# Optimization experiments

Measured on AMD Instinct MI355X. Metric: run time of the kernel, lower is better.

## Reference

```python
import jax, jax.numpy as jnp
import numpy as np

B, N, L = 16, 512, 512          # batch, compound atoms, protein words
DIM = 10                         # compound feature dim
DM, H, DK, DFF = 128, 8, 16, 512 # transformer dims
LG, LO = 3, 3                    # layer_gnn, layer_output
NFP, NW = 10000, 10000           # vocab sizes
NEG = -9e15                      # GAT mask sentinel (matches torch code)


def _layernorm(x, g, b, eps=1e-6):
    # annotated-transformer LayerNorm: unbiased std, eps added to std
    m = jnp.mean(x, -1, keepdims=True)
    s = jnp.std(x, -1, keepdims=True, ddof=1)
    return g * (x - m) / (s + eps) + b


def _pos_encoding(length, d_model):
    pos = np.arange(length)[:, None]
    div = np.exp(np.arange(0, d_model, 2) * (-np.log(10000.0) / d_model))
    pe = np.zeros((length, d_model), np.float32)
    pe[:, 0::2] = np.sin(pos * div)
    pe[:, 1::2] = np.cos(pos * div)
    return jnp.asarray(pe)


def setup_inputs():
    ks = iter(jax.random.split(jax.random.key(0), 64))
    def nrm(shape, scale):
        return jax.random.normal(next(ks), shape, jnp.float32) * scale
    return dict(
        fingerprints=jax.random.randint(next(ks), (B, N), 0, NFP, jnp.int32),
        fp_mask=jnp.ones((B, N), jnp.float32),
        adjacency=jax.random.randint(next(ks), (B, N, N), 0, 2, jnp.int32),
        words=jax.random.randint(next(ks), (B, L), 0, NW, jnp.int32),
        words_mask=jnp.ones((B, L), jnp.float32),
        emb_fp=nrm((NFP, DIM), 0.1),
        emb_word=nrm((NW, DM), 0.1),
        Wg=nrm((LG, DIM, DIM), 0.3), bg=jnp.zeros((LG, DIM), jnp.float32),
        attn_a=nrm((LG, 2 * DIM), 0.3),
        Wq=nrm((DM, DM), 0.09), bq=jnp.zeros((DM,), jnp.float32),
        Wk=nrm((DM, DM), 0.09), bk=jnp.zeros((DM,), jnp.float32),
        Wv=nrm((DM, DM), 0.09), bv=jnp.zeros((DM,), jnp.float32),
        Wo=nrm((DM, DM), 0.09), bo=jnp.zeros((DM,), jnp.float32),
        ln1_g=jnp.ones((DM,), jnp.float32), ln1_b=jnp.zeros((DM,), jnp.float32),
        ln2_g=jnp.ones((DM,), jnp.float32), ln2_b=jnp.zeros((DM,), jnp.float32),
        lnf_g=jnp.ones((DM,), jnp.float32), lnf_b=jnp.zeros((DM,), jnp.float32),
        W1=nrm((DM, DFF), 0.09), b1=jnp.zeros((DFF,), jnp.float32),
        W2=nrm((DFF, DM), 0.045), b2=jnp.zeros((DM,), jnp.float32),
        Wtout=nrm((DM, DIM), 0.09), btout=jnp.zeros((DIM,), jnp.float32),
        Watt=nrm((DIM, DIM), 0.3), batt=jnp.zeros((DIM,), jnp.float32),
        Wout=nrm((LO, 2 * DIM, 2 * DIM), 0.2), bout=jnp.zeros((LO, 2 * DIM), jnp.float32),
        Wint=nrm((2 * DIM, 2), 0.2), bint=jnp.zeros((2,), jnp.float32),
    )


def _forward(fingerprints, fp_mask, adjacency, words, words_mask,
             emb_fp, emb_word, Wg, bg, attn_a,
             Wq, bq, Wk, bk, Wv, bv, Wo, bo,
             ln1_g, ln1_b, ln2_g, ln2_b, lnf_g, lnf_b,
             W1, b1, W2, b2, Wtout, btout,
             Watt, batt, Wout, bout, Wint, bint):
    # ---- GAT over compound graph (dropout disabled = eval/deterministic) ----
    xs = emb_fp[fingerprints]                     # [B,N,DIM]
    mask = fp_mask[:, :, None]                    # [B,N,1]
    adj = adjacency > 0
    for i in range(LG):
        h = jax.nn.relu(xs @ Wg[i] + bg[i]) * mask
        # e[b,i,j] = leaky_relu(a1.h_i + a2.h_j)  == leaky_relu([h_i||h_j] @ a)
        s1 = h @ attn_a[i, :DIM]                  # [B,N]
        s2 = h @ attn_a[i, DIM:]                  # [B,N]
        e = jax.nn.leaky_relu(s1[:, :, None] + s2[:, None, :])  # [B,N,N]
        att = jax.nn.softmax(jnp.where(adj, e, NEG), axis=2)
        xs = xs + att @ h
    compound = jnp.mean(xs * mask, axis=1, keepdims=True)       # [B,1,DIM]

    # ---- transformer encoder, 1 layer, annotated-transformer (pre-norm) ----
    x = emb_word[words] * jnp.sqrt(jnp.float32(DM)) + _pos_encoding(L, DM)
    m4 = words_mask[:, None, None, :] > 0         # [B,1,1,L]
    xn = _layernorm(x, ln1_g, ln1_b)
    heads = lambda t: t.reshape(B, L, H, DK).transpose(0, 2, 1, 3)
    q, k, v = heads(xn @ Wq + bq), heads(xn @ Wk + bk), heads(xn @ Wv + bv)
    scores = jnp.einsum('bhqd,bhkd->bhqk', q, k) / jnp.sqrt(jnp.float32(DK))
    p = jax.nn.softmax(jnp.where(m4, scores, -1e9), axis=-1)
    attn = jnp.einsum('bhqk,bhkd->bhqd', p, v).transpose(0, 2, 1, 3).reshape(B, L, DM)
    x = x + (attn @ Wo + bo)
    xn = _layernorm(x, ln2_g, ln2_b)
    x = x + (jax.nn.relu(xn @ W1 + b1) @ W2 + b2)
    x = _layernorm(x, lnf_g, lnf_b)
    word_vectors = jax.nn.relu(x) @ Wtout + btout  # [B,L,DIM]

    # ---- tanh cross-attention (attention_cnn) ----
    hc = jax.nn.relu(compound @ Watt + batt)       # [B,1,DIM]
    hp = jax.nn.relu(word_vectors @ Watt + batt)   # [B,L,DIM]
    w = jnp.tanh(jnp.einsum('bxd,bld->bxl', hc, hp))  # [B,1,L]
    protein = jnp.mean(w.transpose(0, 2, 1) * hp, axis=1, keepdims=True)  # [B,1,DIM]

    cat = jnp.concatenate([compound, protein], axis=2)  # [B,1,2*DIM]
    for j in range(LO):
        cat = jax.nn.relu(cat @ Wout[j] + bout[j])
    return jnp.squeeze(cat @ Wint + bint, axis=1)        # [B,2]


def reference(fingerprints, fp_mask, adjacency, words, words_mask,
              emb_fp, emb_word, Wg, bg, attn_a,
              Wq, bq, Wk, bk, Wv, bv, Wo, bo,
              ln1_g, ln1_b, ln2_g, ln2_b, lnf_g, lnf_b,
              W1, b1, W2, b2, Wtout, btout,
              Watt, batt, Wout, bout, Wint, bint):
    return _forward(fingerprints, fp_mask, adjacency, words, words_mask,
                    emb_fp, emb_word, Wg, bg, attn_a,
                    Wq, bq, Wk, bk, Wv, bv, Wo, bo,
                    ln1_g, ln1_b, ln2_g, ln2_b, lnf_g, lnf_b,
                    W1, b1, W2, b2, Wtout, btout,
                    Watt, batt, Wout, bout, Wint, bint)
```

## Files before the change

kernel.cpp:

```cpp
#include <hip/hip_runtime.h>
#include <hip/hip_bf16.h>
#include <math.h>

#define B 16
#define N 512
#define L 512
#define DIM 10
#define DM 128
#define H 8
#define DK 16
#define DFF 512
#define LG 3
#define LO 3
#define NEGV -9.0e15f
#define RF 16
#define AQR 64

__device__ __forceinline__ float wave_reduce_sum(float v) {
    #pragma unroll
    for (int o = 32; o > 0; o >>= 1) v += __shfl_down(v, o, 64);
    return v;
}

__device__ __forceinline__ float quad_sum(float x) {
    int y1 = __builtin_amdgcn_mov_dpp(__float_as_int(x), 0xB1, 0xF, 0xF, true);
    float s = x + __int_as_float(y1);
    int y2 = __builtin_amdgcn_mov_dpp(__float_as_int(s), 0x4E, 0xF, 0xF, true);
    return s + __int_as_float(y2);
}

__device__ __forceinline__ float half_reduce_sum(float v) {
    #pragma unroll
    for (int o = 16; o > 0; o >>= 1) v += __shfl_xor(v, o, 64);
    return v;
}


__global__ void k_embed_fp(const int* __restrict__ fing, const float* __restrict__ emb_fp,
                           float* __restrict__ xs) {
    int idx = blockIdx.x * blockDim.x + threadIdx.x;
    if (idx >= B * N * DIM) return;
    int d = idx % DIM;
    int bn = idx / DIM;
    xs[idx] = emb_fp[fing[bn] * DIM + d];
}

__global__ void k_gnn_h(const float* __restrict__ xs, const float* __restrict__ fp_mask,
                        const float* __restrict__ Wg, const float* __restrict__ bg,
                        const float* __restrict__ aatt,
                        float* __restrict__ h, float* __restrict__ s1, float* __restrict__ s2) {
    int bn = blockIdx.x * blockDim.x + threadIdx.x;
    if (bn >= B * N) return;
    float x[DIM];
    #pragma unroll
    for (int d = 0; d < DIM; d++) x[d] = xs[bn * DIM + d];
    float m = fp_mask[bn];
    float a1 = 0.f, a2 = 0.f;
    #pragma unroll
    for (int j = 0; j < DIM; j++) {
        float acc = bg[j];
        #pragma unroll
        for (int d = 0; d < DIM; d++) acc += x[d] * Wg[d * DIM + j];
        acc = fmaxf(acc, 0.f) * m;
        h[bn * DIM + j] = acc;
        a1 += acc * aatt[j];
        a2 += acc * aatt[DIM + j];
    }
    s1[bn] = a1;
    s2[bn] = a2;
}

__global__ void k_gnn_att(const float* __restrict__ h, const float* __restrict__ s1,
                          const float* __restrict__ s2, const int* __restrict__ adj,
                          float* __restrict__ xs) {
    int b  = blockIdx.x / (N / 16);
    int rg = blockIdx.x % (N / 16);
    int t = threadIdx.x;
    int g  = t >> 4;
    int ll = t & 15;
    int i = rg * 16 + g;

    __shared__ float h_s[N * DIM];
    __shared__ float s2_s[N];

    const float* hb = h + (long)b * N * DIM;
    for (int idx = t; idx < N * DIM; idx += 256) h_s[idx] = hb[idx];
    for (int j = t; j < N; j += 256) s2_s[j] = s2[b * N + j];
    __syncthreads();

    float s1v = s1[b * N + i];
    const int* adjrow = adj + ((long)b * N + i) * N;

    float e[32];
    #pragma unroll
    for (int c = 0; c < 32; c++) {
        int j = c * 16 + ll;
        float xsc = s1v + s2_s[j];
        xsc = xsc > 0.f ? xsc : 0.01f * xsc;
        e[c] = (adjrow[j] > 0) ? xsc : NEGV;
    }
    float m = e[0];
    #pragma unroll
    for (int c = 1; c < 32; c++) m = fmaxf(m, e[c]);
    #pragma unroll
    for (int off = 1; off < 16; off <<= 1) m = fmaxf(m, __shfl_xor(m, off, 64));

    float sum = 0.f;
    float a[DIM];
    #pragma unroll
    for (int d = 0; d < DIM; d++) a[d] = 0.f;
    #pragma unroll
    for (int c = 0; c < 32; c++) {
        float p = expf(e[c] - m);
        sum += p;
        int j = c * 16 + ll;
        #pragma unroll
        for (int d = 0; d < DIM; d++) a[d] += p * h_s[j * DIM + d];
    }
    #pragma unroll
    for (int off = 1; off < 16; off <<= 1) {
        sum += __shfl_xor(sum, off, 64);
        #pragma unroll
        for (int d = 0; d < DIM; d++) a[d] += __shfl_xor(a[d], off, 64);
    }
    if (ll < DIM) {
        float av = a[0];
        if (ll == 1) av = a[1]; else if (ll == 2) av = a[2]; else if (ll == 3) av = a[3];
        else if (ll == 4) av = a[4]; else if (ll == 5) av = a[5]; else if (ll == 6) av = a[6];
        else if (ll == 7) av = a[7]; else if (ll == 8) av = a[8]; else if (ll == 9) av = a[9];
        xs[((long)b * N + i) * DIM + ll] += av / sum;
    }
}

__global__ void k_compound(const float* __restrict__ xs, const float* __restrict__ fp_mask,
                           const float* __restrict__ Watt, const float* __restrict__ batt,
                           float* __restrict__ compound, float* __restrict__ hc) {
    int b = blockIdx.x;
    int t = threadIdx.x;
    int wid = t >> 6, lane = t & 63;
    float lacc[DIM];
    #pragma unroll
    for (int d = 0; d < DIM; d++) lacc[d] = 0.f;
    for (int n = t; n < N; n += 256) {
        float m = fp_mask[b * N + n];
        #pragma unroll
        for (int d = 0; d < DIM; d++) lacc[d] += xs[((long)b * N + n) * DIM + d] * m;
    }
    __shared__ float red[4][DIM];
    __shared__ float comp_s[DIM];
    #pragma unroll
    for (int d = 0; d < DIM; d++) lacc[d] = wave_reduce_sum(lacc[d]);
    if (lane == 0) {
        #pragma unroll
        for (int d = 0; d < DIM; d++) red[wid][d] = lacc[d];
    }
    __syncthreads();
    if (t < DIM) {
        float c = (red[0][t] + red[1][t] + red[2][t] + red[3][t]) / (float)N;
        compound[b * DIM + t] = c;
        comp_s[t] = c;
    }
    __syncthreads();
    if (t < DIM) {
        float acc = batt[t];
        #pragma unroll
        for (int e = 0; e < DIM; e++) acc += comp_s[e] * Watt[e * DIM + t];
        hc[b * DIM + t] = fmaxf(acc, 0.f);
    }
}


__global__ void k_pe(float* __restrict__ pe) {
    int idx = blockIdx.x * blockDim.x + threadIdx.x;
    if (idx >= L * DM) return;
    int d = idx % DM, l = idx / DM;
    int k = d >> 1;
    double div = exp((double)(2 * k) * (-log(10000.0) / (double)DM));
    double ang = (double)l * div;
    pe[idx] = (d & 1) ? (float)cos(ang) : (float)sin(ang);
}

__global__ void k_embed_ln(const int* __restrict__ words, const float* __restrict__ emb,
                           const float* __restrict__ pe, const float* __restrict__ g,
                           const float* __restrict__ bb,
                           float* __restrict__ x, float* __restrict__ xn) {
    int row = blockIdx.x;
    int t = threadIdx.x;
    int wid = t >> 6, lane = t & 63;
    int l = row % L;
    float v = emb[(long)words[row] * DM + t] * sqrtf(128.0f) + pe[l * DM + t];
    x[(long)row * DM + t] = v;
    float s = wave_reduce_sum(v);
    __shared__ float r2[2], r3[2];
    if (lane == 0) r2[wid] = s;
    __syncthreads();
    float mean = (r2[0] + r2[1]) / (float)DM;
    float dv = v - mean;
    float q = wave_reduce_sum(dv * dv);
    if (lane == 0) r3[wid] = q;
    __syncthreads();
    float sd = sqrtf((r3[0] + r3[1]) / (float)(DM - 1)) + 1e-6f;
    xn[(long)row * DM + t] = g[t] * dv / sd + bb[t];
}

__global__ void k_qkv(const float* __restrict__ xn,
                      const float* __restrict__ Wq, const float* __restrict__ bq,
                      const float* __restrict__ Wk, const float* __restrict__ bk,
                      const float* __restrict__ Wv, const float* __restrict__ bv,
                      float* __restrict__ q, float* __restrict__ k, float* __restrict__ v) {
    long row0 = (long)blockIdx.x * RF;
    int t = threadIdx.x;
    __shared__ float xs_s[RF * DM];
    for (int i = t; i < RF * DM; i += 384) xs_s[i] = xn[row0 * DM + i];
    __syncthreads();
    int proj = t / DM;
    int j = t % DM;
    const float* W    = proj == 0 ? Wq : (proj == 1 ? Wk : Wv);
    const float* bias = proj == 0 ? bq : (proj == 1 ? bk : bv);
    float* out        = proj == 0 ? q  : (proj == 1 ? k  : v);
    float acc[RF];
    #pragma unroll
    for (int r = 0; r < RF; r++) acc[r] = bias[j];
    for (int d4 = 0; d4 < DM / 4; d4++) {
        float w0 = W[(4 * d4 + 0) * DM + j];
        float w1 = W[(4 * d4 + 1) * DM + j];
        float w2 = W[(4 * d4 + 2) * DM + j];
        float w3 = W[(4 * d4 + 3) * DM + j];
        #pragma unroll
        for (int r = 0; r < RF; r++) {
            float4 xv = ((const float4*)&xs_s[r * DM])[d4];
            acc[r] += xv.x * w0 + xv.y * w1 + xv.z * w2 + xv.w * w3;
        }
    }
    #pragma unroll
    for (int r = 0; r < RF; r++) {
        long row = row0 + r;
        int b = (int)(row / L), l = (int)(row % L);
        out[(((long)b * H + j / DK) * L + l) * DK + (j % DK)] = acc[r];
    }
}

__global__ void __launch_bounds__(256, 4)
k_attn(const float* __restrict__ q, const float* __restrict__ k,
       const float* __restrict__ v, const float* __restrict__ wmask,
       float* __restrict__ attnout) {
    int blk = blockIdx.x;
    int qc = blk % (L / AQR);
    int bh = blk / (L / AQR);
    int b = bh / H, hh = bh % H;
    int t = threadIdx.x;
    int sl = t & 3;
    int r = t >> 2;
    int l = qc * AQR + r;

    __shared__ float4 k_s[L * 4];
    __shared__ float wm_s[L];
    const float4* kb4 = (const float4*)(k + (long)bh * L * DK);
    for (int i = t; i < L * 4; i += 256) k_s[i] = kb4[i];
    for (int j = t; j < L; j += 256) wm_s[j] = (wmask[b * L + j] > 0.f) ? 0.f : -1e9f;
    __syncthreads();

    float4 qr = ((const float4*)(q + ((long)bh * L + l) * DK))[sl];
    qr.x *= 0.25f; qr.y *= 0.25f; qr.z *= 0.25f; qr.w *= 0.25f;

    const float4* vb4 = (const float4*)(v + (long)bh * L * DK);

    float m = -1e30f, ssum = 0.f;
    float4 acc = make_float4(0.f, 0.f, 0.f, 0.f);

    for (int c = 0; c < L / 8; c++) {
        int j0 = c * 8;
        float s8[8];
        #pragma unroll
        for (int jj = 0; jj < 8; jj++) {
            float4 kk = k_s[(j0 + jj) * 4 + sl];
            float part = qr.x * kk.x + qr.y * kk.y + qr.z * kk.z + qr.w * kk.w;
            s8[jj] = quad_sum(part);
        }
        const float4* mp = (const float4*)&wm_s[j0];
        float4 ma = mp[0], mb = mp[1];
        s8[0] += ma.x; s8[1] += ma.y; s8[2] += ma.z; s8[3] += ma.w;
        s8[4] += mb.x; s8[5] += mb.y; s8[6] += mb.z; s8[7] += mb.w;

        float cm = fmaxf(fmaxf(fmaxf(s8[0], s8[1]), fmaxf(s8[2], s8[3])),
                         fmaxf(fmaxf(s8[4], s8[5]), fmaxf(s8[6], s8[7])));
        float mn = fmaxf(m, cm);
        float scale = __expf(m - mn);
        ssum *= scale;
        acc.x *= scale; acc.y *= scale; acc.z *= scale; acc.w *= scale;
        m = mn;
        #pragma unroll
        for (int jj = 0; jj < 8; jj++) {
            float p = __expf(s8[jj] - m);
            ssum += p;
            float4 vv = vb4[(j0 + jj) * 4 + sl];
            acc.x += p * vv.x; acc.y += p * vv.y; acc.z += p * vv.z; acc.w += p * vv.w;
        }
    }

    float inv = 1.f / ssum;
    float4* outp = (float4*)(attnout + ((long)b * L + l) * DM + hh * DK);
    outp[sl] = make_float4(acc.x * inv, acc.y * inv, acc.z * inv, acc.w * inv);
}

__global__ void k_oproj(const float* __restrict__ attnout, const float* __restrict__ Wo,
                        const float* __restrict__ bo, float* __restrict__ x) {
    long row0 = (long)blockIdx.x * RF;
    int t = threadIdx.x;
    __shared__ float a_s[RF * DM];
    for (int i = t; i < RF * DM; i += 128) a_s[i] = attnout[row0 * DM + i];
    __syncthreads();
    float acc[RF];
    #pragma unroll
    for (int r = 0; r < RF; r++) acc[r] = bo[t];
    for (int d4 = 0; d4 < DM / 4; d4++) {
        float w0 = Wo[(4 * d4 + 0) * DM + t];
        float w1 = Wo[(4 * d4 + 1) * DM + t];
        float w2 = Wo[(4 * d4 + 2) * DM + t];
        float w3 = Wo[(4 * d4 + 3) * DM + t];
        #pragma unroll
        for (int r = 0; r < RF; r++) {
            float4 av = ((const float4*)&a_s[r * DM])[d4];
            acc[r] += av.x * w0 + av.y * w1 + av.z * w2 + av.w * w3;
        }
    }
    #pragma unroll
    for (int r = 0; r < RF; r++) x[(row0 + r) * DM + t] += acc[r];
}

__global__ void k_ffn_fused(const float* __restrict__ x,
                            const float* __restrict__ ln2_g, const float* __restrict__ ln2_b,
                            const float* __restrict__ W1, const float* __restrict__ b1,
                            const float* __restrict__ W2, const float* __restrict__ b2,
                            const float* __restrict__ lnf_g, const float* __restrict__ lnf_b,
                            const float* __restrict__ Wtout, const float* __restrict__ btout,
                            const float* __restrict__ Watt, const float* __restrict__ batt,
                            float* __restrict__ hp) {
    long row0 = (long)blockIdx.x * RF;
    int t = threadIdx.x;

    __shared__ float x_s[RF][DM];
    __shared__ float xn_s[RF][DM];
    __shared__ float h_s[RF][DFF];
    __shared__ float r_s[RF][DM + 4];
    __shared__ float wt_s[DM * DIM];
    __shared__ float wa_s[DIM * DIM];
    __shared__ float bt_s[DIM], ba_s[DIM];
    __shared__ float wv_s[RF][DIM];

    {
        float4 xv = ((const float4*)(x + row0 * DM))[t];
        ((float4*)&x_s[0][0])[t] = xv;
        for (int i = t; i < DM * DIM; i += 512) wt_s[i] = Wtout[i];
        for (int i = t; i < DIM * DIM; i += 512) wa_s[i] = Watt[i];
        if (t < DIM) { bt_s[t] = btout[t]; ba_s[t] = batt[t]; }
    }
    __syncthreads();

    {
        int row = t >> 5, c = t & 31;
        float4 v = ((const float4*)&x_s[row][0])[c];
        float s = half_reduce_sum(v.x + v.y + v.z + v.w);
        float mean = s / (float)DM;
        float4 dv = make_float4(v.x - mean, v.y - mean, v.z - mean, v.w - mean);
        float q = half_reduce_sum(dv.x * dv.x + dv.y * dv.y + dv.z * dv.z + dv.w * dv.w);
        float sd = sqrtf(q / (float)(DM - 1)) + 1e-6f;
        const float4 g4 = ((const float4*)ln2_g)[c];
        const float4 b4 = ((const float4*)ln2_b)[c];
        ((float4*)&xn_s[row][0])[c] = make_float4(
            g4.x * dv.x / sd + b4.x, g4.y * dv.y / sd + b4.y,
            g4.z * dv.z / sd + b4.z, g4.w * dv.w / sd + b4.w);
    }
    __syncthreads();

    {
        float acc[RF];
        #pragma unroll
        for (int r = 0; r < RF; r++) acc[r] = b1[t];
        for (int d4 = 0; d4 < DM / 4; d4++) {
            float w0 = W1[(4 * d4 + 0) * DFF + t];
            float w1 = W1[(4 * d4 + 1) * DFF + t];
            float w2 = W1[(4 * d4 + 2) * DFF + t];
            float w3 = W1[(4 * d4 + 3) * DFF + t];
            #pragma unroll
            for (int r = 0; r < RF; r++) {
                float4 xv = ((const float4*)&xn_s[r][0])[d4];
                acc[r] += xv.x * w0 + xv.y * w1 + xv.z * w2 + xv.w * w3;
            }
        }
        #pragma unroll
        for (int r = 0; r < RF; r++) h_s[r][t] = fmaxf(acc[r], 0.f);
    }
    __syncthreads();

    {
        int col = t & 127, rq = t >> 7;
        float acc2[4];
        #pragma unroll
        for (int rr = 0; rr < 4; rr++) acc2[rr] = b2[col];
        for (int f4 = 0; f4 < DFF / 4; f4++) {
            float w0 = W2[(4 * f4 + 0) * DM + col];
            float w1 = W2[(4 * f4 + 1) * DM + col];
            float w2 = W2[(4 * f4 + 2) * DM + col];
            float w3 = W2[(4 * f4 + 3) * DM + col];
            #pragma unroll
            for (int rr = 0; rr < 4; rr++) {
                float4 hv = ((const float4*)&h_s[rq * 4 + rr][0])[f4];
                acc2[rr] += hv.x * w0 + hv.y * w1 + hv.z * w2 + hv.w * w3;
            }
        }
        __syncthreads();
        #pragma unroll
        for (int rr = 0; rr < 4; rr++) {
            int row = rq * 4 + rr;
            xn_s[row][col] = x_s[row][col] + acc2[rr];
        }
    }
    __syncthreads();

    {
        int row = t >> 5, c = t & 31;
        float4 v = ((const float4*)&xn_s[row][0])[c];
        float s = half_reduce_sum(v.x + v.y + v.z + v.w);
        float mean = s / (float)DM;
        float4 dv = make_float4(v.x - mean, v.y - mean, v.z - mean, v.w - mean);
        float q = half_reduce_sum(dv.x * dv.x + dv.y * dv.y + dv.z * dv.z + dv.w * dv.w);
        float sd = sqrtf(q / (float)(DM - 1)) + 1e-6f;
        const float4 g4 = ((const float4*)lnf_g)[c];
        const float4 b4 = ((const float4*)lnf_b)[c];
        r_s[row][4 * c + 0] = fmaxf(g4.x * dv.x / sd + b4.x, 0.f);
        r_s[row][4 * c + 1] = fmaxf(g4.y * dv.y / sd + b4.y, 0.f);
        r_s[row][4 * c + 2] = fmaxf(g4.z * dv.z / sd + b4.z, 0.f);
        r_s[row][4 * c + 3] = fmaxf(g4.w * dv.w / sd + b4.w, 0.f);
    }
    __syncthreads();

    if (t < RF * DIM) {
        int row = t / DIM, o = t % DIM;
        float acc = bt_s[o];
        for (int d = 0; d < DM; d++) acc += r_s[row][d] * wt_s[d * DIM + o];
        wv_s[row][o] = acc;
    }
    __syncthreads();

    if (t < RF * DIM) {
        int row = t / DIM, o = t % DIM;
        float acc = ba_s[o];
        #pragma unroll
        for (int e = 0; e < DIM; e++) acc += wv_s[row][e] * wa_s[e * DIM + o];
        hp[(row0 + row) * DIM + o] = fmaxf(acc, 0.f);
    }
}

__global__ void k_final(const float* __restrict__ hp, const float* __restrict__ hc,
                        const float* __restrict__ compound, const float* __restrict__ Wout,
                        const float* __restrict__ bout, const float* __restrict__ Wint,
                        const float* __restrict__ bint, float* __restrict__ out) {
    int b = blockIdx.x;
    int t = threadIdx.x;
    int wid = t >> 6, lane = t & 63;

    __shared__ float wout_s[LO * 2 * DIM * 2 * DIM];
    __shared__ float bout_s[LO * 2 * DIM];
    __shared__ float wint_s[2 * DIM * 2];
    __shared__ float bint_s[2];
    __shared__ float hc_s[DIM];
    __shared__ float red[4][DIM];
    __shared__ float cat_s[2 * DIM];
    __shared__ float tmp_s[2 * DIM];

    for (int i = t; i < LO * 2 * DIM * 2 * DIM; i += 256) wout_s[i] = Wout[i];
    for (int i = t; i < LO * 2 * DIM; i += 256) bout_s[i] = bout[i];
    for (int i = t; i < 2 * DIM * 2; i += 256) wint_s[i] = Wint[i];
    if (t < 2) bint_s[t] = bint[t];
    if (t < DIM) hc_s[t] = hc[b * DIM + t];
    __syncthreads();

    float lacc[DIM];
    #pragma unroll
    for (int e = 0; e < DIM; e++) lacc[e] = 0.f;
    for (int l = t; l < L; l += 256) {
        const float* hpl = hp + ((long)b * L + l) * DIM;
        float hv[DIM];
        float dot = 0.f;
        #pragma unroll
        for (int e = 0; e < DIM; e++) { hv[e] = hpl[e]; dot += hc_s[e] * hv[e]; }
        float w = tanhf(dot);
        #pragma unroll
        for (int e = 0; e < DIM; e++) lacc[e] += w * hv[e];
    }
    #pragma unroll
    for (int e = 0; e < DIM; e++) lacc[e] = wave_reduce_sum(lacc[e]);
    if (lane == 0) {
        #pragma unroll
        for (int e = 0; e < DIM; e++) red[wid][e] = lacc[e];
    }
    __syncthreads();
    if (t < DIM) {
        cat_s[t] = compound[b * DIM + t];
        cat_s[DIM + t] = (red[0][t] + red[1][t] + red[2][t] + red[3][t]) / (float)L;
    }
    __syncthreads();

    for (int j = 0; j < LO; j++) {
        float acc = 0.f;
        if (t < 2 * DIM) {
            acc = bout_s[j * 2 * DIM + t];
            #pragma unroll
            for (int e = 0; e < 2 * DIM; e++)
                acc += cat_s[e] * wout_s[j * 2 * DIM * 2 * DIM + e * 2 * DIM + t];
            acc = fmaxf(acc, 0.f);
            tmp_s[t] = acc;
        }
        __syncthreads();
        if (t < 2 * DIM) cat_s[t] = tmp_s[t];
        __syncthreads();
    }
    if (t < 2) {
        float o = bint_s[t];
        #pragma unroll
        for (int e = 0; e < 2 * DIM; e++) o += cat_s[e] * wint_s[e * 2 + t];
        out[b * 2 + t] = o;
    }
}

extern "C" void kernel_launch(void* const* d_in, const int* in_sizes, int n_in,
                              void* d_out, int out_size, void* d_ws, size_t ws_size,
                              hipStream_t stream) {
    (void)in_sizes; (void)n_in; (void)out_size; (void)ws_size;
    const int*   fingerprints = (const int*)d_in[0];
    const float* fp_mask      = (const float*)d_in[1];
    const int*   adjacency    = (const int*)d_in[2];
    const int*   words        = (const int*)d_in[3];
    const float* words_mask   = (const float*)d_in[4];
    const float* emb_fp       = (const float*)d_in[5];
    const float* emb_word     = (const float*)d_in[6];
    const float* Wg   = (const float*)d_in[7];
    const float* bg   = (const float*)d_in[8];
    const float* attn_a = (const float*)d_in[9];
    const float* Wq = (const float*)d_in[10];
    const float* bq = (const float*)d_in[11];
    const float* Wk = (const float*)d_in[12];
    const float* bk = (const float*)d_in[13];
    const float* Wv = (const float*)d_in[14];
    const float* bv = (const float*)d_in[15];
    const float* Wo = (const float*)d_in[16];
    const float* bo = (const float*)d_in[17];
    const float* ln1_g = (const float*)d_in[18];
    const float* ln1_b = (const float*)d_in[19];
    const float* ln2_g = (const float*)d_in[20];
    const float* ln2_b = (const float*)d_in[21];
    const float* lnf_g = (const float*)d_in[22];
    const float* lnf_b = (const float*)d_in[23];
    const float* W1 = (const float*)d_in[24];
    const float* b1 = (const float*)d_in[25];
    const float* W2 = (const float*)d_in[26];
    const float* b2 = (const float*)d_in[27];
    const float* Wtout = (const float*)d_in[28];
    const float* btout = (const float*)d_in[29];
    const float* Watt  = (const float*)d_in[30];
    const float* batt  = (const float*)d_in[31];
    const float* Wout  = (const float*)d_in[32];
    const float* bout  = (const float*)d_in[33];
    const float* Wint  = (const float*)d_in[34];
    const float* bint  = (const float*)d_in[35];
    float* out = (float*)d_out;

    float* w = (float*)d_ws;
    float* xs = w;        w += B * N * DIM;
    float* h  = w;        w += B * N * DIM;
    float* s1 = w;        w += B * N;
    float* s2 = w;        w += B * N;
    float* compound = w;  w += B * DIM;
    float* hc = w;        w += B * DIM;
    float* pe = w;        w += L * DM;
    float* x  = w;        w += (long)B * L * DM;
    float* xn = w;        w += (long)B * L * DM;
    float* qb = w;        w += (long)B * H * L * DK;
    float* kb = w;        w += (long)B * H * L * DK;
    float* vb = w;        w += (long)B * H * L * DK;
    float* attnout = w;   w += (long)B * L * DM;
    float* hp = w;        w += (long)B * L * DIM;

    k_embed_fp<<<(B * N * DIM + 255) / 256, 256, 0, stream>>>(fingerprints, emb_fp, xs);
    for (int i = 0; i < LG; i++) {
        k_gnn_h<<<(B * N + 255) / 256, 256, 0, stream>>>(
            xs, fp_mask, Wg + i * DIM * DIM, bg + i * DIM, attn_a + i * 2 * DIM, h, s1, s2);
        k_gnn_att<<<B * (N / 16), 256, 0, stream>>>(h, s1, s2, adjacency, xs);
    }
    k_compound<<<B, 256, 0, stream>>>(xs, fp_mask, Watt, batt, compound, hc);

    k_pe<<<(L * DM + 255) / 256, 256, 0, stream>>>(pe);
    k_embed_ln<<<B * L, DM, 0, stream>>>(words, emb_word, pe, ln1_g, ln1_b, x, xn);
    k_qkv<<<B * L / RF, 3 * DM, 0, stream>>>(xn, Wq, bq, Wk, bk, Wv, bv, qb, kb, vb);
    k_attn<<<B * H * (L / AQR), 256, 0, stream>>>(qb, kb, vb, words_mask, attnout);
    k_oproj<<<B * L / RF, DM, 0, stream>>>(attnout, Wo, bo, x);
    k_ffn_fused<<<B * L / RF, DFF, 0, stream>>>(x, ln2_g, ln2_b, W1, b1, W2, b2,
                                                lnf_g, lnf_b, Wtout, btout, Watt, batt, hp);
    k_final<<<B, 256, 0, stream>>>(hp, hc, compound, Wout, bout, Wint, bint, out);
}
```

Before: 246.3 us.

## Fuse GNN stages, embedding+LN into QKV, output projection into FFN, retile attention

Merges the fingerprint embedding, GNN linear and attention steps into one kernel per layer. Each block recomputes h/s1/s2 for its whole batch in shared memory, and the compound sum is folded into the last layer via atomics. The word embedding and LayerNorm move into the QKV kernel, and the output projection moves into the FFN kernel, which removes the xn buffer and two launches. The attention kernel now uses two lanes per query row instead of four, with 128 rows per block. The cost is redundant per-block GNN recomputation, fewer attention blocks, and nondeterministic atomic ordering.

```diff
diff --git a/kernel.cpp b/kernel.cpp
--- a/kernel.cpp
+++ b/kernel.cpp
@@ -14,7 +14,6 @@
 #define LO 3
 #define NEGV -9.0e15f
 #define RF 16
-#define AQR 64
 
 __device__ __forceinline__ float wave_reduce_sum(float v) {
     #pragma unroll
@@ -22,57 +21,18 @@
     return v;
 }
 
-__device__ __forceinline__ float quad_sum(float x) {
-    int y1 = __builtin_amdgcn_mov_dpp(__float_as_int(x), 0xB1, 0xF, 0xF, true);
-    float s = x + __int_as_float(y1);
-    int y2 = __builtin_amdgcn_mov_dpp(__float_as_int(s), 0x4E, 0xF, 0xF, true);
-    return s + __int_as_float(y2);
-}
-
-__device__ __forceinline__ float half_reduce_sum(float v) {
-    #pragma unroll
-    for (int o = 16; o > 0; o >>= 1) v += __shfl_xor(v, o, 64);
-    return v;
-}
-
-
-__global__ void k_embed_fp(const int* __restrict__ fing, const float* __restrict__ emb_fp,
-                           float* __restrict__ xs) {
-    int idx = blockIdx.x * blockDim.x + threadIdx.x;
-    if (idx >= B * N * DIM) return;
-    int d = idx % DIM;
-    int bn = idx / DIM;
-    xs[idx] = emb_fp[fing[bn] * DIM + d];
-}
-
-__global__ void k_gnn_h(const float* __restrict__ xs, const float* __restrict__ fp_mask,
-                        const float* __restrict__ Wg, const float* __restrict__ bg,
-                        const float* __restrict__ aatt,
-                        float* __restrict__ h, float* __restrict__ s1, float* __restrict__ s2) {
-    int bn = blockIdx.x * blockDim.x + threadIdx.x;
-    if (bn >= B * N) return;
-    float x[DIM];
-    #pragma unroll
-    for (int d = 0; d < DIM; d++) x[d] = xs[bn * DIM + d];
-    float m = fp_mask[bn];
-    float a1 = 0.f, a2 = 0.f;
-    #pragma unroll
-    for (int j = 0; j < DIM; j++) {
-        float acc = bg[j];
-        #pragma unroll
-        for (int d = 0; d < DIM; d++) acc += x[d] * Wg[d * DIM + j];
-        acc = fmaxf(acc, 0.f) * m;
-        h[bn * DIM + j] = acc;
-        a1 += acc * aatt[j];
-        a2 += acc * aatt[DIM + j];
-    }
-    s1[bn] = a1;
-    s2[bn] = a2;
-}
-
-__global__ void k_gnn_att(const float* __restrict__ h, const float* __restrict__ s1,
-                          const float* __restrict__ s2, const int* __restrict__ adj,
-                          float* __restrict__ xs) {
+__device__ __forceinline__ float pair_sum(float x) {
+    int y = __builtin_amdgcn_mov_dpp(__float_as_int(x), 0xB1, 0xF, 0xF, true);
+    return x + __int_as_float(y);
+}
+
+__global__ void k_gnn(const int* __restrict__ fing, const float* __restrict__ emb_fp,
+                      const float* __restrict__ xs_in, const float* __restrict__ fp_mask,
+                      const int* __restrict__ adj,
+                      const float* __restrict__ Wg, const float* __restrict__ bg,
+                      const float* __restrict__ aatt,
+                      float* __restrict__ xs_out, float* __restrict__ compound_raw,
+                      int first, int last) {
     int b  = blockIdx.x / (N / 16);
     int rg = blockIdx.x % (N / 16);
     int t = threadIdx.x;
@@ -80,15 +40,46 @@
     int ll = t & 15;
     int i = rg * 16 + g;
 
+    __shared__ float xs_s[N * DIM];
     __shared__ float h_s[N * DIM];
+    __shared__ float s1_s[N];
     __shared__ float s2_s[N];
-
-    const float* hb = h + (long)b * N * DIM;
-    for (int idx = t; idx < N * DIM; idx += 256) h_s[idx] = hb[idx];
-    for (int j = t; j < N; j += 256) s2_s[j] = s2[b * N + j];
-    __syncthreads();
-
-    float s1v = s1[b * N + i];
+    __shared__ float mk_s[N];
+
+    if (first) {
+        for (int idx = t; idx < N * DIM; idx += 256) {
+            int node = idx / DIM, d = idx % DIM;
+            xs_s[idx] = emb_fp[(long)fing[b * N + node] * DIM + d];
+        }
+    } else {
+        const float* src = xs_in + (long)b * N * DIM;
+        for (int idx = t; idx < N * DIM; idx += 256) xs_s[idx] = src[idx];
+    }
+    for (int j = t; j < N; j += 256) mk_s[j] = fp_mask[b * N + j];
+    __syncthreads();
+
+    for (int nn = t; nn < N; nn += 256) {
+        float x[DIM];
+        #pragma unroll
+        for (int d = 0; d < DIM; d++) x[d] = xs_s[nn * DIM + d];
+        float mk = mk_s[nn];
+        float a1 = 0.f, a2 = 0.f;
+        #pragma unroll
+        for (int j = 0; j < DIM; j++) {
+            float acc = bg[j];
+            #pragma unroll
+            for (int d = 0; d < DIM; d++) acc += x[d] * Wg[d * DIM + j];
+            acc = fmaxf(acc, 0.f) * mk;
+            h_s[nn * DIM + j] = acc;
+            a1 += acc * aatt[j];
+            a2 += acc * aatt[DIM + j];
+        }
+        s1_s[nn] = a1;
+        s2_s[nn] = a2;
+    }
+    __syncthreads();
+
+    float s1v = s1_s[i];
     const int* adjrow = adj + ((long)b * N + i) * N;
 
     float e[32];
@@ -128,44 +119,9 @@
         if (ll == 1) av = a[1]; else if (ll == 2) av = a[2]; else if (ll == 3) av = a[3];
         else if (ll == 4) av = a[4]; else if (ll == 5) av = a[5]; else if (ll == 6) av = a[6];
         else if (ll == 7) av = a[7]; else if (ll == 8) av = a[8]; else if (ll == 9) av = a[9];
-        xs[((long)b * N + i) * DIM + ll] += av / sum;
-    }
-}
-
-__global__ void k_compound(const float* __restrict__ xs, const float* __restrict__ fp_mask,
-                           const float* __restrict__ Watt, const float* __restrict__ batt,
-                           float* __restrict__ compound, float* __restrict__ hc) {
-    int b = blockIdx.x;
-    int t = threadIdx.x;
-    int wid = t >> 6, lane = t & 63;
-    float lacc[DIM];
-    #pragma unroll
-    for (int d = 0; d < DIM; d++) lacc[d] = 0.f;
-    for (int n = t; n < N; n += 256) {
-        float m = fp_mask[b * N + n];
-        #pragma unroll
-        for (int d = 0; d < DIM; d++) lacc[d] += xs[((long)b * N + n) * DIM + d] * m;
-    }
-    __shared__ float red[4][DIM];
-    __shared__ float comp_s[DIM];
-    #pragma unroll
-    for (int d = 0; d < DIM; d++) lacc[d] = wave_reduce_sum(lacc[d]);
-    if (lane == 0) {
-        #pragma unroll
-        for (int d = 0; d < DIM; d++) red[wid][d] = lacc[d];
-    }
-    __syncthreads();
-    if (t < DIM) {
-        float c = (red[0][t] + red[1][t] + red[2][t] + red[3][t]) / (float)N;
-        compound[b * DIM + t] = c;
-        comp_s[t] = c;
-    }
-    __syncthreads();
-    if (t < DIM) {
-        float acc = batt[t];
-        #pragma unroll
-        for (int e = 0; e < DIM; e++) acc += comp_s[e] * Watt[e * DIM + t];
-        hc[b * DIM + t] = fmaxf(acc, 0.f);
+        float newv = xs_s[i * DIM + ll] + av / sum;
+        if (!last) xs_out[((long)b * N + i) * DIM + ll] = newv;
+        else       atomicAdd(&compound_raw[b * DIM + ll], newv * mk_s[i]);
     }
 }
 
@@ -180,39 +136,54 @@
     pe[idx] = (d & 1) ? (float)cos(ang) : (float)sin(ang);
 }
 
-__global__ void k_embed_ln(const int* __restrict__ words, const float* __restrict__ emb,
-                           const float* __restrict__ pe, const float* __restrict__ g,
-                           const float* __restrict__ bb,
-                           float* __restrict__ x, float* __restrict__ xn) {
-    int row = blockIdx.x;
-    int t = threadIdx.x;
-    int wid = t >> 6, lane = t & 63;
-    int l = row % L;
-    float v = emb[(long)words[row] * DM + t] * sqrtf(128.0f) + pe[l * DM + t];
-    x[(long)row * DM + t] = v;
-    float s = wave_reduce_sum(v);
-    __shared__ float r2[2], r3[2];
-    if (lane == 0) r2[wid] = s;
-    __syncthreads();
-    float mean = (r2[0] + r2[1]) / (float)DM;
-    float dv = v - mean;
-    float q = wave_reduce_sum(dv * dv);
-    if (lane == 0) r3[wid] = q;
-    __syncthreads();
-    float sd = sqrtf((r3[0] + r3[1]) / (float)(DM - 1)) + 1e-6f;
-    xn[(long)row * DM + t] = g[t] * dv / sd + bb[t];
-}
-
-__global__ void k_qkv(const float* __restrict__ xn,
+__global__ void k_qkv(const int* __restrict__ words, const float* __restrict__ emb,
+                      const float* __restrict__ pe,
+                      const float* __restrict__ ln1_g, const float* __restrict__ ln1_b,
                       const float* __restrict__ Wq, const float* __restrict__ bq,
                       const float* __restrict__ Wk, const float* __restrict__ bk,
                       const float* __restrict__ Wv, const float* __restrict__ bv,
+                      float* __restrict__ x,
                       float* __restrict__ q, float* __restrict__ k, float* __restrict__ v) {
     long row0 = (long)blockIdx.x * RF;
     int t = threadIdx.x;
-    __shared__ float xs_s[RF * DM];
-    for (int i = t; i < RF * DM; i += 384) xs_s[i] = xn[row0 * DM + i];
-    __syncthreads();
+    __shared__ float x_s[RF * DM];
+    __shared__ float xn_s[RF * DM];
+
+    for (int i = t; i < RF * DM; i += 384) {
+        int row = i >> 7, d = i & 127;
+        long gr = row0 + row;
+        int l = (int)(gr & (L - 1));
+        float val = emb[(long)words[gr] * DM + d] * sqrtf(128.0f) + pe[l * DM + d];
+        x_s[i] = val;
+        x[gr * DM + d] = val;
+    }
+    __syncthreads();
+
+    if (t < 256) {
+        int row = t >> 4, ll = t & 15;
+        float4 v1 = ((const float4*)&x_s[row * DM])[ll * 2];
+        float4 v2 = ((const float4*)&x_s[row * DM])[ll * 2 + 1];
+        float s = v1.x + v1.y + v1.z + v1.w + v2.x + v2.y + v2.z + v2.w;
+        #pragma unroll
+        for (int off = 1; off < 16; off <<= 1) s += __shfl_xor(s, off, 64);
+        float mean = s / (float)DM;
+        float d0 = v1.x - mean, d1 = v1.y - mean, d2 = v1.z - mean, d3 = v1.w - mean;
+        float d4 = v2.x - mean, d5 = v2.y - mean, d6 = v2.z - mean, d7 = v2.w - mean;
+        float qq = d0*d0 + d1*d1 + d2*d2 + d3*d3 + d4*d4 + d5*d5 + d6*d6 + d7*d7;
+        #pragma unroll
+        for (int off = 1; off < 16; off <<= 1) qq += __shfl_xor(qq, off, 64);
+        float sd = sqrtf(qq / (float)(DM - 1)) + 1e-6f;
+        const float4 g1 = ((const float4*)ln1_g)[ll * 2], g2 = ((const float4*)ln1_g)[ll * 2 + 1];
+        const float4 b1 = ((const float4*)ln1_b)[ll * 2], b2 = ((const float4*)ln1_b)[ll * 2 + 1];
+        ((float4*)&xn_s[row * DM])[ll * 2] = make_float4(
+            g1.x * d0 / sd + b1.x, g1.y * d1 / sd + b1.y,
+            g1.z * d2 / sd + b1.z, g1.w * d3 / sd + b1.w);
+        ((float4*)&xn_s[row * DM])[ll * 2 + 1] = make_float4(
+            g2.x * d4 / sd + b2.x, g2.y * d5 / sd + b2.y,
+            g2.z * d6 / sd + b2.z, g2.w * d7 / sd + b2.w);
+    }
+    __syncthreads();
+
     int proj = t / DM;
     int j = t % DM;
     const float* W    = proj == 0 ? Wq : (proj == 1 ? Wk : Wv);
@@ -228,7 +199,7 @@
         float w3 = W[(4 * d4 + 3) * DM + j];
         #pragma unroll
         for (int r = 0; r < RF; r++) {
-            float4 xv = ((const float4*)&xs_s[r * DM])[d4];
+            float4 xv = ((const float4*)&xn_s[r * DM])[d4];
             acc[r] += xv.x * w0 + xv.y * w1 + xv.z * w2 + xv.w * w3;
         }
     }
@@ -245,13 +216,13 @@
        const float* __restrict__ v, const float* __restrict__ wmask,
        float* __restrict__ attnout) {
     int blk = blockIdx.x;
-    int qc = blk % (L / AQR);
-    int bh = blk / (L / AQR);
+    int qc = blk % (L / 128);
+    int bh = blk / (L / 128);
     int b = bh / H, hh = bh % H;
     int t = threadIdx.x;
-    int sl = t & 3;
-    int r = t >> 2;
-    int l = qc * AQR + r;
+    int sl = t & 1;
+    int r = t >> 1;
+    int l = qc * 128 + r;
 
     __shared__ float4 k_s[L * 4];
     __shared__ float wm_s[L];
@@ -260,22 +231,26 @@
     for (int j = t; j < L; j += 256) wm_s[j] = (wmask[b * L + j] > 0.f) ? 0.f : -1e9f;
     __syncthreads();
 
-    float4 qr = ((const float4*)(q + ((long)bh * L + l) * DK))[sl];
-    qr.x *= 0.25f; qr.y *= 0.25f; qr.z *= 0.25f; qr.w *= 0.25f;
+    const float4* qp = (const float4*)(q + ((long)bh * L + l) * DK);
+    float4 qa = qp[sl * 2], qb = qp[sl * 2 + 1];
+    qa.x *= 0.25f; qa.y *= 0.25f; qa.z *= 0.25f; qa.w *= 0.25f;
+    qb.x *= 0.25f; qb.y *= 0.25f; qb.z *= 0.25f; qb.w *= 0.25f;
 
     const float4* vb4 = (const float4*)(v + (long)bh * L * DK);
 
     float m = -1e30f, ssum = 0.f;
-    float4 acc = make_float4(0.f, 0.f, 0.f, 0.f);
+    float4 a0 = make_float4(0.f, 0.f, 0.f, 0.f), a1 = a0;
 
     for (int c = 0; c < L / 8; c++) {
         int j0 = c * 8;
         float s8[8];
         #pragma unroll
         for (int jj = 0; jj < 8; jj++) {
-            float4 kk = k_s[(j0 + jj) * 4 + sl];
-            float part = qr.x * kk.x + qr.y * kk.y + qr.z * kk.z + qr.w * kk.w;
-            s8[jj] = quad_sum(part);
+            float4 ka = k_s[(j0 + jj) * 4 + sl * 2];
+            float4 kb_ = k_s[(j0 + jj) * 4 + sl * 2 + 1];
+            float part = qa.x * ka.x + qa.y * ka.y + qa.z * ka.z + qa.w * ka.w
+                       + qb.x * kb_.x + qb.y * kb_.y + qb.z * kb_.z + qb.w * kb_.w;
+            s8[jj] = pair_sum(part);
         }
         const float4* mp = (const float4*)&wm_s[j0];
         float4 ma = mp[0], mb = mp[1];
@@ -287,48 +262,28 @@
         float mn = fmaxf(m, cm);
         float scale = __expf(m - mn);
         ssum *= scale;
-        acc.x *= scale; acc.y *= scale; acc.z *= scale; acc.w *= scale;
+        a0.x *= scale; a0.y *= scale; a0.z *= scale; a0.w *= scale;
+        a1.x *= scale; a1.y *= scale; a1.z *= scale; a1.w *= scale;
         m = mn;
         #pragma unroll
         for (int jj = 0; jj < 8; jj++) {
             float p = __expf(s8[jj] - m);
             ssum += p;
-            float4 vv = vb4[(j0 + jj) * 4 + sl];
-            acc.x += p * vv.x; acc.y += p * vv.y; acc.z += p * vv.z; acc.w += p * vv.w;
+            float4 va = vb4[(j0 + jj) * 4 + sl * 2];
+            float4 vb2 = vb4[(j0 + jj) * 4 + sl * 2 + 1];
+            a0.x += p * va.x;  a0.y += p * va.y;  a0.z += p * va.z;  a0.w += p * va.w;
+            a1.x += p * vb2.x; a1.y += p * vb2.y; a1.z += p * vb2.z; a1.w += p * vb2.w;
         }
     }
 
     float inv = 1.f / ssum;
     float4* outp = (float4*)(attnout + ((long)b * L + l) * DM + hh * DK);
-    outp[sl] = make_float4(acc.x * inv, acc.y * inv, acc.z * inv, acc.w * inv);
-}
-
-__global__ void k_oproj(const float* __restrict__ attnout, const float* __restrict__ Wo,
-                        const float* __restrict__ bo, float* __restrict__ x) {
-    long row0 = (long)blockIdx.x * RF;
-    int t = threadIdx.x;
-    __shared__ float a_s[RF * DM];
-    for (int i = t; i < RF * DM; i += 128) a_s[i] = attnout[row0 * DM + i];
-    __syncthreads();
-    float acc[RF];
-    #pragma unroll
-    for (int r = 0; r < RF; r++) acc[r] = bo[t];
-    for (int d4 = 0; d4 < DM / 4; d4++) {
-        float w0 = Wo[(4 * d4 + 0) * DM + t];
-        float w1 = Wo[(4 * d4 + 1) * DM + t];
-        float w2 = Wo[(4 * d4 + 2) * DM + t];
-        float w3 = Wo[(4 * d4 + 3) * DM + t];
-        #pragma unroll
-        for (int r = 0; r < RF; r++) {
-            float4 av = ((const float4*)&a_s[r * DM])[d4];
-            acc[r] += av.x * w0 + av.y * w1 + av.z * w2 + av.w * w3;
-        }
-    }
-    #pragma unroll
-    for (int r = 0; r < RF; r++) x[(row0 + r) * DM + t] += acc[r];
-}
-
-__global__ void k_ffn_fused(const float* __restrict__ x,
+    outp[sl * 2]     = make_float4(a0.x * inv, a0.y * inv, a0.z * inv, a0.w * inv);
+    outp[sl * 2 + 1] = make_float4(a1.x * inv, a1.y * inv, a1.z * inv, a1.w * inv);
+}
+
+__global__ void k_ffn_fused(const float* __restrict__ x, const float* __restrict__ attnout,
+                            const float* __restrict__ Wo, const float* __restrict__ bo,
                             const float* __restrict__ ln2_g, const float* __restrict__ ln2_b,
                             const float* __restrict__ W1, const float* __restrict__ b1,
                             const float* __restrict__ W2, const float* __restrict__ b2,
@@ -348,9 +303,10 @@
     __shared__ float bt_s[DIM], ba_s[DIM];
     __shared__ float wv_s[RF][DIM];
 
+    float* a_f = &h_s[0][0];
     {
-        float4 xv = ((const float4*)(x + row0 * DM))[t];
-        ((float4*)&x_s[0][0])[t] = xv;
+        ((float4*)&x_s[0][0])[t] = ((const float4*)(x + row0 * DM))[t];
+        ((float4*)a_f)[t] = ((const float4*)(attnout + row0 * DM))[t];
         for (int i = t; i < DM * DIM; i += 512) wt_s[i] = Wtout[i];
         for (int i = t; i < DIM * DIM; i += 512) wa_s[i] = Watt[i];
         if (t < DIM) { bt_s[t] = btout[t]; ba_s[t] = batt[t]; }
@@ -358,12 +314,40 @@
     __syncthreads();
 
     {
+        int col = t & 127, rq = t >> 7;
+        float acc2[4];
+        #pragma unroll
+        for (int rr = 0; rr < 4; rr++) acc2[rr] = bo[col];
+        for (int d4 = 0; d4 < DM / 4; d4++) {
+            float w0 = Wo[(4 * d4 + 0) * DM + col];
+            float w1 = Wo[(4 * d4 + 1) * DM + col];
+            float w2 = Wo[(4 * d4 + 2) * DM + col];
+            float w3 = Wo[(4 * d4 + 3) * DM + col];
+            #pragma unroll
+            for (int rr = 0; rr < 4; rr++) {
+                float4 av = ((const float4*)&a_f[(rq * 4 + rr) * DM])[d4];
+                acc2[rr] += av.x * w0 + av.y * w1 + av.z * w2 + av.w * w3;
+            }
+        }
+        #pragma unroll
+        for (int rr = 0; rr < 4; rr++) {
+            int row = rq * 4 + rr;
+            x_s[row][col] += acc2[rr];
+        }
+    }
+    __syncthreads();
+
+    {
         int row = t >> 5, c = t & 31;
         float4 v = ((const float4*)&x_s[row][0])[c];
-        float s = half_reduce_sum(v.x + v.y + v.z + v.w);
+        float s = v.x + v.y + v.z + v.w;
+        #pragma unroll
+        for (int o = 16; o > 0; o >>= 1) s += __shfl_xor(s, o, 64);
         float mean = s / (float)DM;
         float4 dv = make_float4(v.x - mean, v.y - mean, v.z - mean, v.w - mean);
-        float q = half_reduce_sum(dv.x * dv.x + dv.y * dv.y + dv.z * dv.z + dv.w * dv.w);
+        float q = dv.x * dv.x + dv.y * dv.y + dv.z * dv.z + dv.w * dv.w;
+        #pragma unroll
+        for (int o = 16; o > 0; o >>= 1) q += __shfl_xor(q, o, 64);
         float sd = sqrtf(q / (float)(DM - 1)) + 1e-6f;
         const float4 g4 = ((const float4*)ln2_g)[c];
         const float4 b4 = ((const float4*)ln2_b)[c];
@@ -388,6 +372,7 @@
                 acc[r] += xv.x * w0 + xv.y * w1 + xv.z * w2 + xv.w * w3;
             }
         }
+        __syncthreads();
         #pragma unroll
         for (int r = 0; r < RF; r++) h_s[r][t] = fmaxf(acc[r], 0.f);
     }
@@ -421,10 +406,14 @@
     {
         int row = t >> 5, c = t & 31;
         float4 v = ((const float4*)&xn_s[row][0])[c];
-        float s = half_reduce_sum(v.x + v.y + v.z + v.w);
+        float s = v.x + v.y + v.z + v.w;
+        #pragma unroll
+        for (int o = 16; o > 0; o >>= 1) s += __shfl_xor(s, o, 64);
         float mean = s / (float)DM;
         float4 dv = make_float4(v.x - mean, v.y - mean, v.z - mean, v.w - mean);
-        float q = half_reduce_sum(dv.x * dv.x + dv.y * dv.y + dv.z * dv.z + dv.w * dv.w);
+        float q = dv.x * dv.x + dv.y * dv.y + dv.z * dv.z + dv.w * dv.w;
+        #pragma unroll
+        for (int o = 16; o > 0; o >>= 1) q += __shfl_xor(q, o, 64);
         float sd = sqrtf(q / (float)(DM - 1)) + 1e-6f;
         const float4 g4 = ((const float4*)lnf_g)[c];
         const float4 b4 = ((const float4*)lnf_b)[c];
@@ -452,10 +441,11 @@
     }
 }
 
-__global__ void k_final(const float* __restrict__ hp, const float* __restrict__ hc,
-                        const float* __restrict__ compound, const float* __restrict__ Wout,
-                        const float* __restrict__ bout, const float* __restrict__ Wint,
-                        const float* __restrict__ bint, float* __restrict__ out) {
+__global__ void k_final(const float* __restrict__ hp, const float* __restrict__ compound_raw,
+                        const float* __restrict__ Watt, const float* __restrict__ batt,
+                        const float* __restrict__ Wout, const float* __restrict__ bout,
+                        const float* __restrict__ Wint, const float* __restrict__ bint,
+                        float* __restrict__ out) {
     int b = blockIdx.x;
     int t = threadIdx.x;
     int wid = t >> 6, lane = t & 63;
@@ -464,6 +454,7 @@
     __shared__ float bout_s[LO * 2 * DIM];
     __shared__ float wint_s[2 * DIM * 2];
     __shared__ float bint_s[2];
+    __shared__ float comp_s[DIM];
     __shared__ float hc_s[DIM];
     __shared__ float red[4][DIM];
     __shared__ float cat_s[2 * DIM];
@@ -473,7 +464,14 @@
     for (int i = t; i < LO * 2 * DIM; i += 256) bout_s[i] = bout[i];
     for (int i = t; i < 2 * DIM * 2; i += 256) wint_s[i] = Wint[i];
     if (t < 2) bint_s[t] = bint[t];
-    if (t < DIM) hc_s[t] = hc[b * DIM + t];
+    if (t < DIM) comp_s[t] = compound_raw[b * DIM + t] * (1.f / (float)N);
+    __syncthreads();
+    if (t < DIM) {
+        float acc = batt[t];
+        #pragma unroll
+        for (int e = 0; e < DIM; e++) acc += comp_s[e] * Watt[e * DIM + t];
+        hc_s[t] = fmaxf(acc, 0.f);
+    }
     __syncthreads();
 
     float lacc[DIM];
@@ -497,7 +495,7 @@
     }
     __syncthreads();
     if (t < DIM) {
-        cat_s[t] = compound[b * DIM + t];
+        cat_s[t] = comp_s[t];
         cat_s[DIM + t] = (red[0][t] + red[1][t] + red[2][t] + red[3][t]) / (float)L;
     }
     __syncthreads();
@@ -567,35 +565,36 @@
     float* out = (float*)d_out;
 
     float* w = (float*)d_ws;
-    float* xs = w;        w += B * N * DIM;
-    float* h  = w;        w += B * N * DIM;
-    float* s1 = w;        w += B * N;
-    float* s2 = w;        w += B * N;
-    float* compound = w;  w += B * DIM;
-    float* hc = w;        w += B * DIM;
+    float* xsA = w;       w += B * N * DIM;
+    float* xsB = w;       w += B * N * DIM;
+    float* compound_raw = w; w += B * DIM;
     float* pe = w;        w += L * DM;
     float* x  = w;        w += (long)B * L * DM;
-    float* xn = w;        w += (long)B * L * DM;
     float* qb = w;        w += (long)B * H * L * DK;
     float* kb = w;        w += (long)B * H * L * DK;
     float* vb = w;        w += (long)B * H * L * DK;
     float* attnout = w;   w += (long)B * L * DM;
     float* hp = w;        w += (long)B * L * DIM;
 
-    k_embed_fp<<<(B * N * DIM + 255) / 256, 256, 0, stream>>>(fingerprints, emb_fp, xs);
-    for (int i = 0; i < LG; i++) {
-        k_gnn_h<<<(B * N + 255) / 256, 256, 0, stream>>>(
-            xs, fp_mask, Wg + i * DIM * DIM, bg + i * DIM, attn_a + i * 2 * DIM, h, s1, s2);
-        k_gnn_att<<<B * (N / 16), 256, 0, stream>>>(h, s1, s2, adjacency, xs);
-    }
-    k_compound<<<B, 256, 0, stream>>>(xs, fp_mask, Watt, batt, compound, hc);
+    hipMemsetAsync(compound_raw, 0, B * DIM * sizeof(float), stream);
+
+    k_gnn<<<B * (N / 16), 256, 0, stream>>>(fingerprints, emb_fp, nullptr, fp_mask,
+        adjacency, Wg + 0 * DIM * DIM, bg + 0 * DIM, attn_a + 0 * 2 * DIM,
+        xsA, nullptr, 1, 0);
+    k_gnn<<<B * (N / 16), 256, 0, stream>>>(fingerprints, emb_fp, xsA, fp_mask,
+        adjacency, Wg + 1 * DIM * DIM, bg + 1 * DIM, attn_a + 1 * 2 * DIM,
+        xsB, nullptr, 0, 0);
+    k_gnn<<<B * (N / 16), 256, 0, stream>>>(fingerprints, emb_fp, xsB, fp_mask,
+        adjacency, Wg + 2 * DIM * DIM, bg + 2 * DIM, attn_a + 2 * 2 * DIM,
+        nullptr, compound_raw, 0, 1);
 
     k_pe<<<(L * DM + 255) / 256, 256, 0, stream>>>(pe);
-    k_embed_ln<<<B * L, DM, 0, stream>>>(words, emb_word, pe, ln1_g, ln1_b, x, xn);
-    k_qkv<<<B * L / RF, 3 * DM, 0, stream>>>(xn, Wq, bq, Wk, bk, Wv, bv, qb, kb, vb);
-    k_attn<<<B * H * (L / AQR), 256, 0, stream>>>(qb, kb, vb, words_mask, attnout);
-    k_oproj<<<B * L / RF, DM, 0, stream>>>(attnout, Wo, bo, x);
-    k_ffn_fused<<<B * L / RF, DFF, 0, stream>>>(x, ln2_g, ln2_b, W1, b1, W2, b2,
-                                                lnf_g, lnf_b, Wtout, btout, Watt, batt, hp);
-    k_final<<<B, 256, 0, stream>>>(hp, hc, compound, Wout, bout, Wint, bint, out);
-}
+    k_qkv<<<B * L / RF, 3 * DM, 0, stream>>>(words, emb_word, pe, ln1_g, ln1_b,
+                                             Wq, bq, Wk, bk, Wv, bv, x, qb, kb, vb);
+    k_attn<<<B * H * (L / 128), 256, 0, stream>>>(qb, kb, vb, words_mask, attnout);
+    k_ffn_fused<<<B * L / RF, DFF, 0, stream>>>(x, attnout, Wo, bo, ln2_g, ln2_b,
+                                                W1, b1, W2, b2, lnf_g, lnf_b,
+                                                Wtout, btout, Watt, batt, hp);
+    k_final<<<B, 256, 0, stream>>>(hp, compound_raw, Watt, batt,
+                                   Wout, bout, Wint, bint, out);
+}
```

New measurement: 347.7 us. 41.2% more time.
